# Kernel tuning notes

Measured on AMD Instinct MI355X. Metric: run time of the kernel, lower is better.

The kernel has to match this reference:

```python
import jax, jax.numpy as jnp
import numpy as np

N = 100000      # nodes
E = 3200000     # edges per graph (pos and neg)
IN_FEATS = 128
HIDDEN = 32
PROP_STEP = 8
USE_RELU = False  # args.relu default False


def setup_inputs() -> dict:
    key = jax.random.key(0)
    ks = jax.random.split(key, 8)
    in_feat = jax.random.normal(ks[0], (N, IN_FEATS), dtype=jnp.float32)
    src = jax.random.randint(ks[1], (E,), 0, N, dtype=jnp.int32)
    dst = jax.random.randint(ks[2], (E,), 0, N, dtype=jnp.int32)
    neg_src = jax.random.randint(ks[3], (E,), 0, N, dtype=jnp.int32)
    neg_dst = jax.random.randint(ks[4], (E,), 0, N, dtype=jnp.int32)
    W1 = jax.random.normal(ks[5], (IN_FEATS, HIDDEN), dtype=jnp.float32) * (1.0 / np.sqrt(IN_FEATS))
    b1 = jnp.zeros((HIDDEN,), dtype=jnp.float32)
    gamma = jnp.ones((HIDDEN,), dtype=jnp.float32)
    beta = jnp.zeros((HIDDEN,), dtype=jnp.float32)
    W2 = jax.random.normal(ks[6], (HIDDEN, HIDDEN), dtype=jnp.float32) * (1.0 / np.sqrt(HIDDEN))
    b2 = jnp.zeros((HIDDEN,), dtype=jnp.float32)
    return dict(in_feat=in_feat, W1=W1, b1=b1, gamma=gamma, beta=beta,
                W2=W2, b2=b2, src=src, dst=dst, neg_src=neg_src, neg_dst=neg_dst)


def _graph_conv(h, src, dst, n_nodes):
    """DGL GraphConv(norm='both', weight=False, bias=False):
       out = D_dst^{-1/2} A D_src^{-1/2} h, sum aggregation."""
    ones = jnp.ones(src.shape, dtype=h.dtype)
    out_deg = jax.ops.segment_sum(ones, src, num_segments=n_nodes)
    in_deg = jax.ops.segment_sum(ones, dst, num_segments=n_nodes)
    hs = h * jax.lax.rsqrt(jnp.clip(out_deg, 1.0))[:, None]   # [N, H]
    msg = hs[src]                                             # [E, H] gather
    agg = jax.ops.segment_sum(msg, dst, num_segments=n_nodes)  # [N, H] scatter-add
    return agg * jax.lax.rsqrt(jnp.clip(in_deg, 1.0))[:, None]


def reference(in_feat, W1, b1, gamma, beta, W2, b2, src, dst, neg_src, neg_dst):
    # MLP: Linear -> BatchNorm1d (training-mode batch stats) -> (Dropout noop) -> ReLU -> Linear
    x = in_feat @ W1 + b1
    mu = jnp.mean(x, axis=0)
    var = jnp.var(x, axis=0)
    x = (x - mu) * jax.lax.rsqrt(var + 1e-5) * gamma + beta
    x = jax.nn.relu(x)
    ori_h = x @ W2 + b2                                       # [N, H]

    # Iterative pos-neg SpMM propagation with residual (h initialized to ori_h)
    h = ori_h
    for _ in range(PROP_STEP):
        if USE_RELU:
            h = jax.nn.relu(h)
        h = _graph_conv(h, src, dst, N) - _graph_conv(h, neg_src, neg_dst, N) + ori_h
    return h
```

## Files before the change

kernel.cpp:

```cpp
#include <hip/hip_runtime.h>
#include <hip/hip_fp16.h>

#define N_NODES 100000
#define E_EDGES 3200000
#define IN_F 128
#define HID 32
#define PROP 8

#define WIN 32768
#define NWIN 4
#define HS 32

#define MB_ROWS 64
#define MB_BLOCKS ((N_NODES + MB_ROWS - 1) / MB_ROWS)
#define RED_B 32

#define FB 512
#define CH 12500
#define BK_SH 7
#define BK_N 128
#define NBK 782
#define L2S (NBK * FB)
#define SCB2 391
#define STG 12288

__global__ __launch_bounds__(256) void hist_kernel(const int* __restrict__ s,
        const int* __restrict__ ns, int* __restrict__ degs) {
    __shared__ int lh[WIN];
    int b = blockIdx.x;
    int w = b % NWIN;
    int st = (b / NWIN) % 2;
    int sl = b / (NWIN * 2);
    const int* p = st ? ns : s;
    for (int i = threadIdx.x; i < WIN; i += 256) lh[i] = 0;
    __syncthreads();
    const int lo = w * WIN;
    const int per = E_EDGES / HS;
    const int4* p4 = (const int4*)(p + sl * per);
    for (int i = threadIdx.x; i < per / 4; i += 256) {
        int4 v = p4[i];
        int a;
        a = v.x - lo; if ((unsigned)a < WIN) atomicAdd(&lh[a], 1);
        a = v.y - lo; if ((unsigned)a < WIN) atomicAdd(&lh[a], 1);
        a = v.z - lo; if ((unsigned)a < WIN) atomicAdd(&lh[a], 1);
        a = v.w - lo; if ((unsigned)a < WIN) atomicAdd(&lh[a], 1);
    }
    __syncthreads();
    int* g = degs + st * N_NODES;
    for (int i = threadIdx.x; i < WIN; i += 256) {
        int idx = lo + i;
        if (idx < N_NODES && lh[i]) atomicAdd(&g[idx], lh[i]);
    }
}

__global__ void inv_sqrt_kernel(const int* __restrict__ deg, float* __restrict__ inv, int n) {
    int i = blockIdx.x * blockDim.x + threadIdx.x;
    if (i < n) inv[i] = rsqrtf(fmaxf((float)deg[i], 1.0f));
}

__global__ __launch_bounds__(256) void countA_kernel(const int* __restrict__ dst,
        const int* __restrict__ ndst, int* __restrict__ counts) {
    __shared__ int lh[NBK];
    int blk = blockIdx.x;
    for (int i = threadIdx.x; i < NBK; i += 256) lh[i] = 0;
    __syncthreads();
    const int* dp = (blk < FB / 2) ? dst + blk * CH : ndst + (blk - FB / 2) * CH;
    const int4* dp4 = (const int4*)dp;
    for (int i = threadIdx.x; i < CH / 4; i += 256) {
        int4 v = dp4[i];
        atomicAdd(&lh[v.x >> BK_SH], 1);
        atomicAdd(&lh[v.y >> BK_SH], 1);
        atomicAdd(&lh[v.z >> BK_SH], 1);
        atomicAdd(&lh[v.w >> BK_SH], 1);
    }
    __syncthreads();
    for (int b = threadIdx.x; b < NBK; b += 256) counts[b * FB + blk] = lh[b];
}

__global__ __launch_bounds__(1024) void scanA2_kernel(const int* __restrict__ counts,
        int* __restrict__ offs, int* __restrict__ blockSums) {
    __shared__ int sh[1024];
    int t = threadIdx.x, b = blockIdx.x;
    int i = b * 1024 + t;
    int v = counts[i];
    sh[t] = v;
    __syncthreads();
    for (int off = 1; off < 1024; off <<= 1) {
        int u = (t >= off) ? sh[t - off] : 0;
        __syncthreads();
        sh[t] += u;
        __syncthreads();
    }
    offs[i] = sh[t] - v;
    if (t == 1023) blockSums[b] = sh[1023];
}

__global__ __launch_bounds__(512) void scanB2_kernel(const int* __restrict__ blockSums,
        int* __restrict__ blockOff) {
    __shared__ int sh[512];
    int t = threadIdx.x;
    int v = (t < SCB2) ? blockSums[t] : 0;
    sh[t] = v;
    __syncthreads();
    for (int off = 1; off < 512; off <<= 1) {
        int u = (t >= off) ? sh[t - off] : 0;
        __syncthreads();
        sh[t] += u;
        __syncthreads();
    }
    if (t < SCB2) blockOff[t] = sh[t] - v;
}

__global__ __launch_bounds__(1024) void scanC2_kernel(int* __restrict__ offs,
        const int* __restrict__ blockOff) {
    int b = blockIdx.x, t = threadIdx.x;
    int i = b * 1024 + t;
    offs[i] += blockOff[b];
    if (i == 0) offs[L2S] = 2 * E_EDGES;
}

__global__ __launch_bounds__(256) void fillA2_kernel(const int* __restrict__ src, const int* __restrict__ dst,
        const int* __restrict__ nsrc, const int* __restrict__ ndst,
        const int* __restrict__ offs, int* __restrict__ rec) {
    __shared__ int cur[NBK];
    __shared__ int base[NBK];
    int blk = blockIdx.x;
    int g = (blk >= FB / 2);
    const int* sp = g ? (nsrc + (blk - FB / 2) * CH) : (src + blk * CH);
    const int* dp = g ? (ndst + (blk - FB / 2) * CH) : (dst + blk * CH);
    const int gbit = g << 24;
    for (int i = threadIdx.x; i < NBK; i += 256) {
        cur[i] = 0;
        base[i] = offs[i * FB + blk];
    }
    __syncthreads();
    for (int i = threadIdx.x; i < CH; i += 256) {
        int u = sp[i], v = dp[i];
        int b = v >> BK_SH;
        int p = base[b] + atomicAdd(&cur[b], 1);
        rec[p] = u | ((v & (BK_N - 1)) << 17) | gbit;
    }
}

__global__ __launch_bounds__(256) void reorder_kernel(const int* __restrict__ offs,
        const int* __restrict__ rec, const float* __restrict__ invs,
        int2* __restrict__ rec2, int* __restrict__ row_ptr2) {
    __shared__ int cnt[BK_N];
    __shared__ int cntp[BK_N];
    __shared__ int scn[BK_N];
    __shared__ int lbase[BK_N];
    __shared__ float invp[BK_N], invn[BK_N];
    __shared__ int2 stage[STG];
    int bkt = blockIdx.x, tid = threadIdx.x;
    if (tid < BK_N) { cnt[tid] = 0; cntp[tid] = 0; }
    __syncthreads();
    int beg = offs[bkt * FB], end = offs[(bkt + 1) * FB];
    for (int i = beg + tid; i < end; i += 256) {
        int rx = rec[i];
        int d = (rx >> 17) & (BK_N - 1);
        atomicAdd(&cnt[d], 1);
        if (!(rx & (1 << 24))) atomicAdd(&cntp[d], 1);
    }
    __syncthreads();
    int v = (tid < BK_N) ? cnt[tid] : 0;
    if (tid < BK_N) {
        scn[tid] = v;
        int np = cntp[tid];
        invp[tid] = rsqrtf(fmaxf((float)np, 1.0f));
        invn[tid] = rsqrtf(fmaxf((float)(v - np), 1.0f));
    }
    __syncthreads();
    for (int off = 1; off < BK_N; off <<= 1) {
        int u = (tid < BK_N && tid >= off) ? scn[tid - off] : 0;
        __syncthreads();
        if (tid < BK_N) scn[tid] += u;
        __syncthreads();
    }
    if (tid < BK_N) {
        int b = scn[tid] - v;
        lbase[tid] = b;
        row_ptr2[bkt * BK_N + tid] = beg + b;
        cnt[tid] = 0;
    }
    if (bkt == NBK - 1 && tid == 0) row_ptr2[NBK * BK_N] = 2 * E_EDGES;
    __syncthreads();
    for (int i = beg + tid; i < end; i += 256) {
        int rx = rec[i];
        int d = (rx >> 17) & (BK_N - 1);
        int g = (rx >> 24) & 1;
        int u = rx & 0x1FFFF;
        float io = invs[u + (g ? N_NODES : 0)];
        float c = (g ? -io : io) * (g ? invn[d] : invp[d]);
        int p = lbase[d] + atomicAdd(&cnt[d], 1);
        stage[p] = make_int2(u, __float_as_int(c));
    }
    __syncthreads();
    int n = end - beg;
    for (int j = tid; j < n; j += 256) rec2[beg + j] = stage[j];
}

__global__ __launch_bounds__(256) void mlp1_kernel(const float* __restrict__ in_feat,
        const float* __restrict__ W1, const float* __restrict__ b1,
        float* __restrict__ x, float* __restrict__ partials) {
    __shared__ float4 sRow4[MB_ROWS * 32];
    __shared__ float  sW1t[32 * 132];
    int tid = threadIdx.x;
    for (int idx = tid; idx < IN_F * HID; idx += 256) {
        int j = idx >> 5, k = idx & 31;
        sW1t[k * 132 + j] = W1[idx];
    }
    int nb = blockIdx.x * MB_ROWS;
    const float4* inf4 = (const float4*)in_feat;
    for (int idx = tid; idx < MB_ROWS * 32; idx += 256) {
        int row = idx >> 5, q = idx & 31;
        int g = nb + row;
        float4 v = (g < N_NODES) ? inf4[(size_t)g * 32 + q] : make_float4(0.f, 0.f, 0.f, 0.f);
        sRow4[row * 32 + (q ^ (row & 31))] = v;
    }
    __syncthreads();
    int rt = tid & 31, kt = tid >> 5;
    int k0 = kt * 4;
    float acc[2][4] = {{0.f}};
    const float4* w0p = (const float4*)&sW1t[(k0 + 0) * 132];
    const float4* w1p = (const float4*)&sW1t[(k0 + 1) * 132];
    const float4* w2p = (const float4*)&sW1t[(k0 + 2) * 132];
    const float4* w3p = (const float4*)&sW1t[(k0 + 3) * 132];
    #pragma unroll 4
    for (int jq = 0; jq < 32; ++jq) {
        int pq = jq ^ rt;
        float4 a0 = sRow4[rt * 32 + pq];
        float4 a1 = sRow4[(rt + 32) * 32 + pq];
        float4 w0 = w0p[jq], w1 = w1p[jq], w2 = w2p[jq], w3 = w3p[jq];
        acc[0][0] += a0.x*w0.x + a0.y*w0.y + a0.z*w0.z + a0.w*w0.w;
        acc[0][1] += a0.x*w1.x + a0.y*w1.y + a0.z*w1.z + a0.w*w1.w;
        acc[0][2] += a0.x*w2.x + a0.y*w2.y + a0.z*w2.z + a0.w*w2.w;
        acc[0][3] += a0.x*w3.x + a0.y*w3.y + a0.z*w3.z + a0.w*w3.w;
        acc[1][0] += a1.x*w0.x + a1.y*w0.y + a1.z*w0.z + a1.w*w0.w;
        acc[1][1] += a1.x*w1.x + a1.y*w1.y + a1.z*w1.z + a1.w*w1.w;
        acc[1][2] += a1.x*w2.x + a1.y*w2.y + a1.z*w2.z + a1.w*w2.w;
        acc[1][3] += a1.x*w3.x + a1.y*w3.y + a1.z*w3.z + a1.w*w3.w;
    }
    float bb[4] = { b1[k0], b1[k0 + 1], b1[k0 + 2], b1[k0 + 3] };
    float s[4] = {0.f, 0.f, 0.f, 0.f}, ss[4] = {0.f, 0.f, 0.f, 0.f};
    #pragma unroll
    for (int i = 0; i < 2; ++i) {
        int row = nb + rt + 32 * i;
        if (row < N_NODES) {
            float4 o;
            o.x = acc[i][0] + bb[0];
            o.y = acc[i][1] + bb[1];
            o.z = acc[i][2] + bb[2];
            o.w = acc[i][3] + bb[3];
            *(float4*)&x[(size_t)row * HID + k0] = o;
            s[0] += o.x; ss[0] += o.x * o.x;
            s[1] += o.y; ss[1] += o.y * o.y;
            s[2] += o.z; ss[2] += o.z * o.z;
            s[3] += o.w; ss[3] += o.w * o.w;
        }
    }
    for (int off = 16; off; off >>= 1) {
        #pragma unroll
        for (int c = 0; c < 4; ++c) {
            s[c]  += __shfl_down(s[c],  off, 32);
            ss[c] += __shfl_down(ss[c], off, 32);
        }
    }
    if (rt == 0) {
        float* pb = partials + (size_t)blockIdx.x * 64;
        #pragma unroll
        for (int c = 0; c < 4; ++c) {
            pb[k0 + c]      = s[c];
            pb[32 + k0 + c] = ss[c];
        }
    }
}

__global__ __launch_bounds__(256) void bnred_kernel(const float* __restrict__ partials,
        float* __restrict__ partials2) {
    __shared__ float red[4][64];
    int t = threadIdx.x, b = blockIdx.x;
    int r = t >> 6, c = t & 63;
    float sum = 0.f;
    for (int g = b * 4 + r; g < MB_BLOCKS; g += RED_B * 4)
        sum += partials[(size_t)g * 64 + c];
    red[r][c] = sum;
    __syncthreads();
    if (t < 64) partials2[b * 64 + t] = (red[0][t] + red[1][t]) + (red[2][t] + red[3][t]);
}

__global__ __launch_bounds__(256) void bnparam_kernel(const float* __restrict__ partials2,
        const float* __restrict__ gamma, const float* __restrict__ beta, float* __restrict__ params) {
    __shared__ float red[4][64];
    int t = threadIdx.x;
    int col = t & 63, ch = t >> 6;
    float sum = 0.f;
    for (int g = ch; g < RED_B; g += 4) sum += partials2[(size_t)g * 64 + col];
    red[ch][col] = sum;
    __syncthreads();
    if (t < 64) red[0][t] = red[0][t] + red[1][t] + red[2][t] + red[3][t];
    __syncthreads();
    if (t < HID) {
        float mu  = red[0][t] * (1.0f / (float)N_NODES);
        float var = red[0][t + 32] * (1.0f / (float)N_NODES) - mu * mu;
        float sg = gamma[t] * rsqrtf(var + 1e-5f);
        params[t]       = sg;
        params[HID + t] = beta[t] - mu * sg;
    }
}

__global__ __launch_bounds__(256) void mlp2_kernel(const float* __restrict__ x,
        const float* __restrict__ params, const float* __restrict__ W2,
        const float* __restrict__ b2, float* __restrict__ ori_h, __half* __restrict__ h16) {
    __shared__ float sW2[HID * HID];
    __shared__ float sXn[8][HID];
    int tid = threadIdx.x;
    for (int i = tid; i < HID * HID; i += 256) sW2[i] = W2[i];
    int nb = blockIdx.x * 8;
    int k = tid & 31, r = tid >> 5;
    float v = x[(size_t)(nb + r) * HID + k];
    v = fmaxf(fmaf(v, params[k], params[HID + k]), 0.f);
    sXn[r][k] = v;
    __syncthreads();
    float acc = b2[k];
    #pragma unroll
    for (int j = 0; j < HID; ++j) acc = fmaf(sXn[r][j], sW2[j * HID + k], acc);
    int o = (nb + r) * HID + k;
    ori_h[o] = acc;
    h16[o] = __float2half(acc);
}

__device__ __forceinline__ float2 h2f(int b) {
    __half2 h; __builtin_memcpy(&h, &b, 4); return __half22float2(h);
}

__global__ __launch_bounds__(256) void gather_kernel(const int* __restrict__ row_ptr,
        const int2* __restrict__ rec, const int4* __restrict__ h4,
        const float4* __restrict__ ori4, int4* __restrict__ hn4, float4* __restrict__ out4) {
    int tid = threadIdx.x;
    int node = blockIdx.x * 8 + (tid >> 5);
    int lane = tid & 31;
    int slot = lane >> 2;
    int ql = lane & 3;
    int beg = row_ptr[node], end = row_ptr[node + 1];
    float2 a0 = {0.f, 0.f}, a1 = {0.f, 0.f}, a2 = {0.f, 0.f}, a3 = {0.f, 0.f};
    int i = beg;
#define ACC8(f, c) { float2 u_; \
        u_ = h2f((f).x); a0.x = fmaf((c), u_.x, a0.x); a0.y = fmaf((c), u_.y, a0.y); \
        u_ = h2f((f).y); a1.x = fmaf((c), u_.x, a1.x); a1.y = fmaf((c), u_.y, a1.y); \
        u_ = h2f((f).z); a2.x = fmaf((c), u_.x, a2.x); a2.y = fmaf((c), u_.y, a2.y); \
        u_ = h2f((f).w); a3.x = fmaf((c), u_.x, a3.x); a3.y = fmaf((c), u_.y, a3.y); }
    for (; i + 32 <= end; i += 32) {
        int2 r0 = rec[i + slot];
        int2 r1 = rec[i + 8 + slot];
        int2 r2 = rec[i + 16 + slot];
        int2 r3 = rec[i + 24 + slot];
        int4 f0 = h4[r0.x * 4 + ql];
        int4 f1 = h4[r1.x * 4 + ql];
        int4 f2 = h4[r2.x * 4 + ql];
        int4 f3 = h4[r3.x * 4 + ql];
        float c0 = __int_as_float(r0.y), c1 = __int_as_float(r1.y);
        float c2 = __int_as_float(r2.y), c3 = __int_as_float(r3.y);
        ACC8(f0, c0) ACC8(f1, c1) ACC8(f2, c2) ACC8(f3, c3)
    }
    for (; i + 8 <= end; i += 8) {
        int2 r = rec[i + slot];
        int4 f = h4[r.x * 4 + ql];
        float c = __int_as_float(r.y);
        ACC8(f, c)
    }
    if (i + slot < end) {
        int2 r = rec[i + slot];
        int4 f = h4[r.x * 4 + ql];
        float c = __int_as_float(r.y);
        ACC8(f, c)
    }
#undef ACC8
    #pragma unroll
    for (int off = 4; off <= 16; off <<= 1) {
        a0.x += __shfl_down(a0.x, off, 32); a0.y += __shfl_down(a0.y, off, 32);
        a1.x += __shfl_down(a1.x, off, 32); a1.y += __shfl_down(a1.y, off, 32);
        a2.x += __shfl_down(a2.x, off, 32); a2.y += __shfl_down(a2.y, off, 32);
        a3.x += __shfl_down(a3.x, off, 32); a3.y += __shfl_down(a3.y, off, 32);
    }
    if (slot == 0) {
        float4 oA = ori4[node * 8 + ql * 2];
        float4 oB = ori4[node * 8 + ql * 2 + 1];
        float r0x = a0.x + oA.x, r0y = a0.y + oA.y;
        float r1x = a1.x + oA.z, r1y = a1.y + oA.w;
        float r2x = a2.x + oB.x, r2y = a2.y + oB.y;
        float r3x = a3.x + oB.z, r3y = a3.y + oB.w;
        if (out4) {
            out4[node * 8 + ql * 2]     = make_float4(r0x, r0y, r1x, r1y);
            out4[node * 8 + ql * 2 + 1] = make_float4(r2x, r2y, r3x, r3y);
        } else {
            __half2 p0 = __floats2half2_rn(r0x, r0y);
            __half2 p1 = __floats2half2_rn(r1x, r1y);
            __half2 p2 = __floats2half2_rn(r2x, r2y);
            __half2 p3 = __floats2half2_rn(r3x, r3y);
            int4 w;
            __builtin_memcpy(&w.x, &p0, 4);
            __builtin_memcpy(&w.y, &p1, 4);
            __builtin_memcpy(&w.z, &p2, 4);
            __builtin_memcpy(&w.w, &p3, 4);
            hn4[node * 4 + ql] = w;
        }
    }
}

extern "C" void kernel_launch(void* const* d_in, const int* in_sizes, int n_in,
                              void* d_out, int out_size, void* d_ws, size_t ws_size,
                              hipStream_t stream) {
    const float* in_feat = (const float*)d_in[0];
    const float* W1    = (const float*)d_in[1];
    const float* b1    = (const float*)d_in[2];
    const float* gamma = (const float*)d_in[3];
    const float* beta  = (const float*)d_in[4];
    const float* W2    = (const float*)d_in[5];
    const float* b2    = (const float*)d_in[6];
    const int* src  = (const int*)d_in[7];
    const int* dst  = (const int*)d_in[8];
    const int* nsrc = (const int*)d_in[9];
    const int* ndst = (const int*)d_in[10];
    float* out = (float*)d_out;

    float* ws      = (float*)d_ws;
    float* x       = ws;
    float* ori_h   = x + (size_t)N_NODES * HID;
    float* invs    = ori_h + (size_t)N_NODES * HID;
    float* params  = invs + 2 * (size_t)N_NODES;
    float* partials= params + 2 * HID;
    float* partials2 = partials + (size_t)MB_BLOCKS * 64;
    int*   degs    = (int*)(partials2 + (size_t)RED_B * 64);
    int*   offs    = degs + 2 * N_NODES;
    int*   blockSums = offs + L2S + 2;
    int*   blockOff  = blockSums + 512;
    int*   row_ptr2  = blockOff + 512;
    uintptr_t hp  = (uintptr_t)(row_ptr2 + NBK * BK_N + 2);
    hp = (hp + 63) & ~(uintptr_t)63;
    __half* h16A   = (__half*)hp;
    __half* h16B   = h16A + (size_t)N_NODES * HID;
    uintptr_t rp  = (uintptr_t)(h16B + (size_t)N_NODES * HID);
    rp = (rp + 63) & ~(uintptr_t)63;
    int*   rec    = (int*)rp;
    int*   counts = (int*)x;
    int2*  rec2   = (int2*)in_feat;

    hipMemsetAsync(degs, 0, 2 * (size_t)N_NODES * sizeof(int), stream);

    hist_kernel<<<NWIN * 2 * HS, 256, 0, stream>>>(src, nsrc, degs);
    inv_sqrt_kernel<<<(2 * N_NODES + 255) / 256, 256, 0, stream>>>(degs, invs, 2 * N_NODES);

    countA_kernel<<<FB, 256, 0, stream>>>(dst, ndst, counts);
    scanA2_kernel<<<SCB2, 1024, 0, stream>>>(counts, offs, blockSums);
    scanB2_kernel<<<1, 512, 0, stream>>>(blockSums, blockOff);
    scanC2_kernel<<<SCB2, 1024, 0, stream>>>(offs, blockOff);
    fillA2_kernel<<<FB, 256, 0, stream>>>(src, dst, nsrc, ndst, offs, rec);

    mlp1_kernel<<<MB_BLOCKS, 256, 0, stream>>>(in_feat, W1, b1, x, partials);
    bnred_kernel<<<RED_B, 256, 0, stream>>>(partials, partials2);
    bnparam_kernel<<<1, 256, 0, stream>>>(partials2, gamma, beta, params);
    mlp2_kernel<<<N_NODES / 8, 256, 0, stream>>>(x, params, W2, b2, ori_h, h16A);

    reorder_kernel<<<NBK, 256, 0, stream>>>(offs, rec, invs, rec2, row_ptr2);

    const __half* h = h16A;
    for (int it = 0; it < PROP; ++it) {
        __half* hn16 = (it & 1) ? h16A : h16B;
        float* o32 = (it == PROP - 1) ? out : nullptr;
        gather_kernel<<<N_NODES / 8, 256, 0, stream>>>(row_ptr2, rec2,
                (const int4*)h, (const float4*)ori_h, (int4*)hn16, (float4*)o32);
        h = hn16;
    }
}
```

Baseline: 980.0 us.

## Split reorder kernel into four sub-blocks per bucket to shrink LDS staging

Each bucket's reorder is now handled by four blocks, each owning 32 of the 128 destination rows. The shared staging buffer drops from 12288 to 3072 int2 entries, and launch bounds request more resident blocks, so occupancy and parallelism rise. In exchange, every sub-block re-reads the whole bucket's records twice (count and scatter) and recomputes the histogram and scan, which multiplies global reads of rec. Staging capacity also shrinks, which relies on each quarter holding at most 3072 edges; the expected count is about 2048.

```diff
diff --git a/kernel.cpp b/kernel.cpp
--- a/kernel.cpp
+++ b/kernel.cpp
@@ -22,7 +22,9 @@
 #define NBK 782
 #define L2S (NBK * FB)
 #define SCB2 391
-#define STG 12288
+#define SPLIT 4
+#define SUBN 32
+#define STG 3072
 
 __global__ __launch_bounds__(256) void hist_kernel(const int* __restrict__ s,
         const int* __restrict__ ns, int* __restrict__ degs) {
@@ -142,16 +144,18 @@
     }
 }
 
-__global__ __launch_bounds__(256) void reorder_kernel(const int* __restrict__ offs,
+__global__ __launch_bounds__(256, 5) void reorder_kernel(const int* __restrict__ offs,
         const int* __restrict__ rec, const float* __restrict__ invs,
         int2* __restrict__ rec2, int* __restrict__ row_ptr2) {
     __shared__ int cnt[BK_N];
     __shared__ int cntp[BK_N];
     __shared__ int scn[BK_N];
-    __shared__ int lbase[BK_N];
+    __shared__ int ex[BK_N];
     __shared__ float invp[BK_N], invn[BK_N];
     __shared__ int2 stage[STG];
-    int bkt = blockIdx.x, tid = threadIdx.x;
+    int blk = blockIdx.x;
+    int bkt = blk >> 2, sub = blk & (SPLIT - 1);
+    int tid = threadIdx.x;
     if (tid < BK_N) { cnt[tid] = 0; cntp[tid] = 0; }
     __syncthreads();
     int beg = offs[bkt * FB], end = offs[(bkt + 1) * FB];
@@ -176,27 +180,32 @@
         if (tid < BK_N) scn[tid] += u;
         __syncthreads();
     }
+    int lo = sub * SUBN, hi = lo + SUBN;
     if (tid < BK_N) {
-        int b = scn[tid] - v;
-        lbase[tid] = b;
-        row_ptr2[bkt * BK_N + tid] = beg + b;
+        ex[tid] = scn[tid] - v;
         cnt[tid] = 0;
-    }
-    if (bkt == NBK - 1 && tid == 0) row_ptr2[NBK * BK_N] = 2 * E_EDGES;
-    __syncthreads();
+        if (tid >= lo && tid < hi)
+            row_ptr2[bkt * BK_N + tid] = beg + ex[tid];
+    }
+    if (bkt == NBK - 1 && sub == SPLIT - 1 && tid == 0)
+        row_ptr2[NBK * BK_N] = 2 * E_EDGES;
+    __syncthreads();
+    int base0 = ex[lo];
+    int base1 = (sub == SPLIT - 1) ? (end - beg) : ex[hi];
     for (int i = beg + tid; i < end; i += 256) {
         int rx = rec[i];
         int d = (rx >> 17) & (BK_N - 1);
+        if (d < lo || d >= hi) continue;
         int g = (rx >> 24) & 1;
         int u = rx & 0x1FFFF;
         float io = invs[u + (g ? N_NODES : 0)];
         float c = (g ? -io : io) * (g ? invn[d] : invp[d]);
-        int p = lbase[d] + atomicAdd(&cnt[d], 1);
+        int p = ex[d] - base0 + atomicAdd(&cnt[d], 1);
         stage[p] = make_int2(u, __float_as_int(c));
     }
     __syncthreads();
-    int n = end - beg;
-    for (int j = tid; j < n; j += 256) rec2[beg + j] = stage[j];
+    int n = base1 - base0;
+    for (int j = tid; j < n; j += 256) rec2[beg + base0 + j] = stage[j];
 }
 
 __global__ __launch_bounds__(256) void mlp1_kernel(const float* __restrict__ in_feat,
@@ -461,7 +470,7 @@
     bnparam_kernel<<<1, 256, 0, stream>>>(partials2, gamma, beta, params);
     mlp2_kernel<<<N_NODES / 8, 256, 0, stream>>>(x, params, W2, b2, ori_h, h16A);
 
-    reorder_kernel<<<NBK, 256, 0, stream>>>(offs, rec, invs, rec2, row_ptr2);
+    reorder_kernel<<<NBK * SPLIT, 256, 0, stream>>>(offs, rec, invs, rec2, row_ptr2);
 
     const __half* h = h16A;
     for (int it = 0; it < PROP; ++it) {
```

Measured after the change: 972.0 us. About the same (-0.8%).
